# Optimization experiments

Measured on AMD Instinct MI355X. Metric: run time of the kernel, lower is better.

Reference implementation:

```python
import jax, jax.numpy as jnp
import numpy as np

N = 192            # image grid size (NxN)
N_SHOTS = 192
N_SAMPLES = 192
TWO_PI = 2.0 * np.pi
PIPE_ITERS = 3     # gpunufft default is ~10; 3 suffices for a CPU-runnable reference


def initialize_2D_radial(n_shots, n_samples):
    """Radial trajectory, k in [-0.5, 0.5), shape (n_shots*n_samples, 2)."""
    angles = np.pi * np.arange(n_shots) / n_shots
    radii = np.linspace(-0.5, 0.5, n_samples, endpoint=False)
    kx = radii[None, :] * np.cos(angles[:, None])
    ky = radii[None, :] * np.sin(angles[:, None])
    return np.stack([kx, ky], axis=-1).reshape(-1, 2).astype(np.float32)


def setup_inputs() -> dict:
    key = jax.random.key(0)
    x = jax.random.normal(key, (2, N, N), dtype=jnp.float32)  # real/imag image
    trajectory = jnp.asarray(initialize_2D_radial(N_SHOTS, N_SAMPLES))  # (M,2)
    return {"x": x, "trajectory": trajectory}


def _mats(traj):
    # Separable NDFT factors: exp(-2pi i k_x * px), exp(-2pi i k_y * py).
    # A: (M, N), B: (M, N); M*N complex64 ~= 57 MB each.
    p = jnp.arange(N, dtype=jnp.float32) - N / 2.0  # centered pixel coords
    A = jnp.exp(-1j * TWO_PI * traj[:, 0:1] * p[None, :])
    B = jnp.exp(-1j * TWO_PI * traj[:, 1:2] * p[None, :])
    return A.astype(jnp.complex64), B.astype(jnp.complex64)


def _op(img, A, B):
    # type-2 NUFFT (exact NDFT): image (N,N) -> kspace (M,)
    t = jnp.einsum('my,xy->mx', B, img)      # contract y first
    return jnp.einsum('mx,mx->m', A, t)


def _adj(d, A, B):
    # type-1 NUFFT adjoint: samples (M,) -> image (N,N)
    return jnp.einsum('mx,my->xy', jnp.conj(A) * d[:, None], jnp.conj(B))


def _pipe_density(A, B):
    # Pipe & Menon iterative density compensation: w <- w / |F F^H w|
    w = jnp.ones(A.shape[0], dtype=jnp.complex64)
    def body(i, w):
        q = _op(_adj(w, A, B), A, B)
        return w / jnp.maximum(jnp.abs(q), 1e-20)
    w = jax.lax.fori_loop(0, PIPE_ITERS, body, w)
    return jnp.abs(w)  # real positive weights


def reference(x, trajectory):
    img = (x[0] + 1j * x[1]).astype(jnp.complex64)  # (N,N) complex image
    A, B = _mats(trajectory)
    # density weights computed from detached trajectory (gpunufft init-time)
    traj_sg = jax.lax.stop_gradient(trajectory)
    Asg, Bsg = _mats(traj_sg)
    w = jax.lax.stop_gradient(_pipe_density(Asg, Bsg))
    kspace = _op(img, A, B)                       # forward NUFFT
    adjoint = _adj(w * kspace, A, B)              # density-compensated adjoint
    return jnp.stack([adjoint.real, adjoint.imag])  # (2,N,N) float32
```

## Files before the change

kernel.cpp:

```cpp
#include <hip/hip_runtime.h>
#include <math.h>


#define MTOT 36864
#define NPIX 192
#define SPLITS 128
#define MPS (MTOT / SPLITS)
#define ADJ_CHUNKS (MPS / 16)
#define PG 4

typedef __attribute__((ext_vector_type(8))) short s16x8;
typedef __attribute__((ext_vector_type(4))) float f32x4;
typedef __attribute__((ext_vector_type(4))) unsigned u32x4;

__device__ __forceinline__ f32x4 mfma_bf16(u32x4 a, u32x4 b, f32x4 c) {
    return __builtin_amdgcn_mfma_f32_16x16x32_bf16(
        __builtin_bit_cast(s16x8, a), __builtin_bit_cast(s16x8, b), c, 0, 0, 0);
}

__device__ __forceinline__ void split_pk(float a, float b, unsigned &hi, unsigned &lo) {
    const unsigned ua = __float_as_uint(a), ub = __float_as_uint(b);
    const unsigned ha = (ua + 0x8000u) & 0xffff0000u;
    const unsigned hb = (ub + 0x8000u) & 0xffff0000u;
    hi = (ha >> 16) | hb;
    const float la = a - __uint_as_float(ha);
    const float lb = b - __uint_as_float(hb);
    lo = ((__float_as_uint(la) + 0x8000u) >> 16) |
         ((__float_as_uint(lb) + 0x8000u) & 0xffff0000u);
}

__device__ __forceinline__ void ksplit(float k, float &kh, float &kl) {
    kh = __uint_as_float(__float_as_uint(k) & 0xfffff000u);
    kl = k - kh;
}
__device__ __forceinline__ float redphase(float kh, float kl, float p) {
    float r = kh * p;
    r -= rintf(r);
    r = fmaf(kl, p, r);
    return r;
}
__device__ __forceinline__ unsigned rot16(unsigned v) {
    return __builtin_amdgcn_alignbit(v, v, 16);
}

__global__ void precompP_k(const float* __restrict__ traj, const int comp,
                           unsigned* __restrict__ PS) {
    const int m = blockIdx.x * 256 + threadIdx.x;
    const int c = blockIdx.y;
    float kh, kl; ksplit(traj[2 * m + comp], kh, kl);
    const float ph = redphase(kh, kl, (float)(c - 96));
    const float co = __builtin_amdgcn_cosf(ph);
    const float si = __builtin_amdgcn_sinf(ph);
    unsigned h, l; split_pk(co, -si, h, l);
    const int mc = m >> 4, mi = m & 15;
    PS[(size_t)mc * 6144 + c * 16 + mi]        = h;
    PS[(size_t)mc * 6144 + 3072 + c * 16 + mi] = l;
}

__global__ void ebuild_k(const float* __restrict__ traj,
                         const float* __restrict__ dr, const float* __restrict__ di,
                         unsigned* __restrict__ ES) {
    const int m = blockIdx.x * 256 + threadIdx.x;
    const int c = blockIdx.y;
    float kh, kl; ksplit(traj[2 * m], kh, kl);
    const float ph = redphase(kh, kl, (float)(c - 96));
    const float co = __builtin_amdgcn_cosf(ph);
    const float si = __builtin_amdgcn_sinf(ph);
    const float dr_ = dr[m], di_ = di[m];
    const float Er = co * dr_ - si * di_;
    const float Ei = co * di_ + si * dr_;
    unsigned h, l; split_pk(Er, Ei, h, l);
    const int mc = m >> 4, mi = m & 15;
    ES[(size_t)mc * 6144 + c * 16 + mi]        = h;
    ES[(size_t)mc * 6144 + 3072 + c * 16 + mi] = l;
}

__global__ void winit_k(float* __restrict__ wr, float* __restrict__ wi) {
    const int m = blockIdx.x * 256 + threadIdx.x;
    wr[m] = 1.f; wi[m] = 0.f;
}

__global__ __launch_bounds__(64, 4) void adj_gemm_k(
    const unsigned* __restrict__ ES, const unsigned* __restrict__ BS,
    float* __restrict__ outP)
{
    const int lane = threadIdx.x & 63;
    const int l15 = lane & 15, qd = lane >> 4;
    const int L = blockIdx.x;
    const int xcd = L & 7, j = L >> 3;
    const int s = xcd * (SPLITS / 8) + j / 36;
    const int r = j % 36;
    const int tile = r >> 2, wid = r & 3;
    const int bx = tile % 3, by = tile / 3;
    const int wi = wid & 1, wj = wid >> 1;
    const int x0 = bx * 64 + wi * 32, y0 = by * 64 + wj * 32;
    float* outRe = outP + (size_t)(s & (PG - 1)) * (2 * MTOT);
    float* outIm = outRe + MTOT;

    const int eo0 = (x0 + l15) * 16 + qd * 4;
    const int eo1 = (x0 + 16 + l15) * 16 + qd * 4;
    const int bo0 = (y0 + l15) * 16 + qd * 4;
    const int bo1 = (y0 + 16 + l15) * 16 + qd * 4;

    const unsigned* Ep = ES + (size_t)(s * ADJ_CHUNKS) * 6144;
    const unsigned* Bp = BS + (size_t)(s * ADJ_CHUNKS) * 6144;

    f32x4 accRe[2][2], accIm[2][2];
    #pragma unroll
    for (int i = 0; i < 2; ++i)
        #pragma unroll
        for (int j2 = 0; j2 < 2; ++j2) {
            accRe[i][j2] = (f32x4){0.f, 0.f, 0.f, 0.f};
            accIm[i][j2] = (f32x4){0.f, 0.f, 0.f, 0.f};
        }

    u32x4 Ra[8], Rb[8];

#define LOADSET(R)                                          \
    R[0] = *(const u32x4*)(Ep + eo0);                       \
    R[1] = *(const u32x4*)(Ep + eo1);                       \
    R[2] = *(const u32x4*)(Ep + 3072 + eo0);                \
    R[3] = *(const u32x4*)(Ep + 3072 + eo1);                \
    R[4] = *(const u32x4*)(Bp + bo0);                       \
    R[5] = *(const u32x4*)(Bp + bo1);                       \
    R[6] = *(const u32x4*)(Bp + 3072 + bo0);                \
    R[7] = *(const u32x4*)(Bp + 3072 + bo1);

#define COMPUTE(R)                                                         \
    {                                                                      \
        _Pragma("unroll")                                                  \
        for (int sj = 0; sj < 2; ++sj) {                                   \
            const u32x4 Ph = R[4 + sj];                                    \
            const u32x4 Pl = R[6 + sj];                                    \
            u32x4 Qh, Ql;                                                  \
            _Pragma("unroll")                                              \
            for (int rr = 0; rr < 4; ++rr) {                               \
                Qh[rr] = rot16(Ph[rr]) ^ 0x00008000u;                      \
                Ql[rr] = rot16(Pl[rr]) ^ 0x00008000u;                      \
            }                                                              \
            _Pragma("unroll")                                              \
            for (int si = 0; si < 2; ++si) {                               \
                const u32x4 Eh = R[si];                                    \
                const u32x4 El = R[2 + si];                                \
                accRe[si][sj] = mfma_bf16(Eh, Ph, accRe[si][sj]);          \
                accRe[si][sj] = mfma_bf16(Eh, Pl, accRe[si][sj]);          \
                accRe[si][sj] = mfma_bf16(El, Ph, accRe[si][sj]);          \
                accIm[si][sj] = mfma_bf16(Eh, Qh, accIm[si][sj]);          \
                accIm[si][sj] = mfma_bf16(Eh, Ql, accIm[si][sj]);          \
                accIm[si][sj] = mfma_bf16(El, Qh, accIm[si][sj]);          \
            }                                                              \
        }                                                                  \
    }

    LOADSET(Ra);
    #pragma unroll 1
    for (int it = 0; it < (ADJ_CHUNKS - 2) / 2; ++it) {
        Ep += 6144; Bp += 6144;
        LOADSET(Rb);
        __builtin_amdgcn_sched_barrier(0);
        COMPUTE(Ra);
        Ep += 6144; Bp += 6144;
        LOADSET(Ra);
        __builtin_amdgcn_sched_barrier(0);
        COMPUTE(Rb);
    }
    Ep += 6144; Bp += 6144;
    LOADSET(Rb);
    __builtin_amdgcn_sched_barrier(0);
    COMPUTE(Ra);
    __builtin_amdgcn_sched_barrier(0);
    COMPUTE(Rb);

#undef LOADSET
#undef COMPUTE

    #pragma unroll
    for (int si = 0; si < 2; ++si)
        #pragma unroll
        for (int sj = 0; sj < 2; ++sj)
            #pragma unroll
            for (int rg = 0; rg < 4; ++rg) {
                const int x = x0 + si * 16 + qd * 4 + rg;
                const int y = y0 + sj * 16 + l15;
                atomicAdd(outRe + x * NPIX + y, accRe[si][sj][rg]);
                atomicAdd(outIm + x * NPIX + y, accIm[si][sj][rg]);
            }
}

__device__ __forceinline__ void fw_stage_load(const unsigned* __restrict__ Ghi,
                                              const unsigned* __restrict__ Glo,
                                              int tid, int koff, u32x4 st[3]) {
    #pragma unroll
    for (int j = 0; j < 3; ++j) {
        const int li = tid + j * 576;
        if (li < 1536) {
            const int row = li >> 3, pl = (li >> 2) & 1, qt = li & 3;
            const unsigned* src = pl ? Glo : Ghi;
            st[j] = *(const u32x4*)(src + row * 192 + koff + qt * 4);
        }
    }
}
__device__ __forceinline__ void fw_stage_write(unsigned* sb, int tid, const u32x4 st[3]) {
    #pragma unroll
    for (int j = 0; j < 3; ++j) {
        const int li = tid + j * 576;
        if (li < 1536) {
            const int row = li >> 3, pl = (li >> 2) & 1, qt = li & 3;
            *(u32x4*)(sb + pl * 3840 + row * 20 + qt * 4) = st[j];
        }
    }
}

__global__ __launch_bounds__(576) void fwdq_k(
    const float* __restrict__ traj,
    const unsigned* __restrict__ Ghi, const unsigned* __restrict__ Glo,
    float* __restrict__ wre, float* __restrict__ wim,
    const int mode,
    float* __restrict__ qre, float* __restrict__ qim)
{
    __shared__ unsigned sG[2][2 * 3840];
    const int tid = threadIdx.x;
    const int lane = tid & 63, wid = tid >> 6;
    const int l15 = lane & 15, q = lane >> 4;
    const int m = (blockIdx.x * 9 + wid) * 16 + l15;
    const float2 kk = *(const float2*)(traj + 2 * m);
    float kxh, kxl, kyh, kyl;
    ksplit(kk.x, kxh, kxl);
    ksplit(kk.y, kyh, kyl);

    f32x4 tre[12], tim[12];
    #pragma unroll
    for (int i = 0; i < 12; ++i) {
        tre[i] = (f32x4){0.f, 0.f, 0.f, 0.f};
        tim[i] = (f32x4){0.f, 0.f, 0.f, 0.f};
    }

    float bc, bs;
    { const float ph = redphase(kyh, kyl, (float)(q * 4 - 96)); 
      bc = __builtin_amdgcn_cosf(ph); bs = __builtin_amdgcn_sinf(ph); }
    const float r1c = __builtin_amdgcn_cosf(kk.y), r1s = __builtin_amdgcn_sinf(kk.y);
    float r16c, r16s;
    { float g = kk.y * 16.f; g -= rintf(g);
      r16c = __builtin_amdgcn_cosf(g); r16s = __builtin_amdgcn_sinf(g); }

    u32x4 st[3];
    fw_stage_load(Ghi, Glo, tid, 0, st);
    fw_stage_write(&sG[0][0], tid, st);
    __syncthreads();

    for (int ch = 0; ch < 12; ++ch) {
        if (ch < 11) fw_stage_load(Ghi, Glo, tid, (ch + 1) * 16, st);

        u32x4 Ph, Pl, Qh, Ql;
        {
            float c = bc, s = bs;
            #pragma unroll
            for (int r = 0; r < 4; ++r) {
                unsigned h, l; split_pk(c, s, h, l);
                Ph[r] = h; Pl[r] = l;
                Qh[r] = rot16(h) ^ 0x00008000u;
                Ql[r] = rot16(l) ^ 0x00008000u;
                const float nc = c * r1c - s * r1s, ns = s * r1c + c * r1s;
                c = nc; s = ns;
            }
            const float nbc = bc * r16c - bs * r16s, nbs = bs * r16c + bc * r16s;
            bc = nbc; bs = nbs;
        }

        const unsigned* sb = &sG[ch & 1][0];
        #pragma unroll
        for (int si = 0; si < 12; ++si) {
            const int base = (si * 16 + l15) * 20 + q * 4;
            const u32x4 gh = *(const u32x4*)(sb + base);
            const u32x4 gl = *(const u32x4*)(sb + 3840 + base);
            tre[si] = mfma_bf16(gh, Ph, tre[si]);
            tre[si] = mfma_bf16(gh, Pl, tre[si]);
            tre[si] = mfma_bf16(gl, Ph, tre[si]);
            tim[si] = mfma_bf16(gh, Qh, tim[si]);
            tim[si] = mfma_bf16(gh, Ql, tim[si]);
            tim[si] = mfma_bf16(gl, Qh, tim[si]);
        }

        if (ch < 11) {
            __syncthreads();
            fw_stage_write(&sG[(ch + 1) & 1][0], tid, st);
            __syncthreads();
        }
    }

    float qr = 0.f, qi = 0.f;
    {
        float g = kk.x * 16.f; g -= rintf(g);
        const float rc = __builtin_amdgcn_cosf(g), rs = __builtin_amdgcn_sinf(g);
        #pragma unroll
        for (int rg = 0; rg < 4; ++rg) {
            const float ph = redphase(kxh, kxl, (float)(q * 4 + rg - 96));
            float c = __builtin_amdgcn_cosf(ph), s = __builtin_amdgcn_sinf(ph);
            #pragma unroll
            for (int si = 0; si < 12; ++si) {
                const float tr = tre[si][rg], ti = tim[si][rg];
                qr += c * tr + s * ti;
                qi += c * ti - s * tr;
                const float nc = c * rc - s * rs, ns = s * rc + c * rs;
                c = nc; s = ns;
            }
        }
    }
    qr += __shfl_xor(qr, 16); qi += __shfl_xor(qi, 16);
    qr += __shfl_xor(qr, 32); qi += __shfl_xor(qi, 32);
    if (lane < 16) {
        if (mode == 0) {
            const float den = fmaxf(sqrtf(qr * qr + qi * qi), 1e-20f);
            wre[m] /= den; wim[m] /= den;
        } else {
            const float sc = sqrtf(wre[m] * wre[m] + wim[m] * wim[m]);
            qre[m] = qr * sc; qim[m] = qi * sc;
        }
    }
}

__global__ void presplit_k(const float* __restrict__ re, const float* __restrict__ im,
                           unsigned* __restrict__ Gh, unsigned* __restrict__ Gl) {
    const int e = blockIdx.x * 256 + threadIdx.x;
    unsigned h, l;
    split_pk(re[e], im[e], h, l);
    Gh[e] = h; Gl[e] = l;
}

__global__ void presplitP_k(const float* __restrict__ outP,
                            unsigned* __restrict__ Gh, unsigned* __restrict__ Gl) {
    const int e = blockIdx.x * 256 + threadIdx.x;
    float re = 0.f, im = 0.f;
    #pragma unroll
    for (int g = 0; g < PG; ++g) {
        re += outP[(size_t)g * (2 * MTOT) + e];
        im += outP[(size_t)g * (2 * MTOT) + MTOT + e];
    }
    unsigned h, l;
    split_pk(re, im, h, l);
    Gh[e] = h; Gl[e] = l;
}

__global__ void reduceOut_k(const float* __restrict__ outP, float* __restrict__ out) {
    const int e = blockIdx.x * 256 + threadIdx.x;
    float re = 0.f, im = 0.f;
    #pragma unroll
    for (int g = 0; g < PG; ++g) {
        re += outP[(size_t)g * (2 * MTOT) + e];
        im += outP[(size_t)g * (2 * MTOT) + MTOT + e];
    }
    out[e] = re; out[MTOT + e] = im;
}

extern "C" void kernel_launch(void* const* d_in, const int* in_sizes, int n_in,
                              void* d_out, int out_size, void* d_ws, size_t ws_size,
                              hipStream_t stream)
{
    const float* xin  = (const float*)d_in[0];
    const float* traj = (const float*)d_in[1];
    float* out = (float*)d_out;

    char* pb = (char*)d_ws;
    unsigned* BS = (unsigned*)pb; pb += (size_t)2304 * 6144 * 4;
    unsigned* ES = (unsigned*)pb; pb += (size_t)2304 * 6144 * 4;
    float* outP = (float*)pb; pb += (size_t)PG * 2 * MTOT * 4;
    float* wr   = (float*)pb; pb += MTOT * 4;
    float* wi   = (float*)pb; pb += MTOT * 4;
    float* dre  = (float*)pb; pb += MTOT * 4;
    float* dim_ = (float*)pb; pb += MTOT * 4;
    unsigned* Ghi = (unsigned*)pb; pb += MTOT * 4;
    unsigned* Glo = (unsigned*)pb; pb += MTOT * 4;

    precompP_k<<<dim3(MTOT / 256, NPIX), 256, 0, stream>>>(traj, 1, BS);
    winit_k<<<MTOT / 256, 256, 0, stream>>>(wr, wi);

    for (int it = 0; it < 3; ++it) {
        hipMemsetAsync(outP, 0, (size_t)PG * 2 * MTOT * 4, stream);
        ebuild_k<<<dim3(MTOT / 256, NPIX), 256, 0, stream>>>(traj, wr, wi, ES);
        adj_gemm_k<<<36 * SPLITS, 64, 0, stream>>>(ES, BS, outP);
        presplitP_k<<<MTOT / 256, 256, 0, stream>>>(outP, Ghi, Glo);
        fwdq_k<<<256, 576, 0, stream>>>(traj, Ghi, Glo, wr, wi, 0, dre, dim_);
    }

    presplit_k<<<MTOT / 256, 256, 0, stream>>>(xin, xin + MTOT, Ghi, Glo);
    fwdq_k<<<256, 576, 0, stream>>>(traj, Ghi, Glo, wr, wi, 1, dre, dim_);
    hipMemsetAsync(outP, 0, (size_t)PG * 2 * MTOT * 4, stream);
    ebuild_k<<<dim3(MTOT / 256, NPIX), 256, 0, stream>>>(traj, dre, dim_, ES);
    adj_gemm_k<<<36 * SPLITS, 64, 0, stream>>>(ES, BS, outP);
    reduceOut_k<<<MTOT / 256, 256, 0, stream>>>(outP, out);
}
```

Measured before the change: 528.3 us.

## Replace adjoint atomics with per-split partial slabs and drop memsets

```diff
diff --git a/kernel.cpp b/kernel.cpp
--- a/kernel.cpp
+++ b/kernel.cpp
@@ -7,7 +7,7 @@
 #define SPLITS 128
 #define MPS (MTOT / SPLITS)
 #define ADJ_CHUNKS (MPS / 16)
-#define PG 4
+#define PG 128
 
 typedef __attribute__((ext_vector_type(8))) short s16x8;
 typedef __attribute__((ext_vector_type(4))) float f32x4;
@@ -94,13 +94,13 @@
     const int bx = tile % 3, by = tile / 3;
     const int wi = wid & 1, wj = wid >> 1;
     const int x0 = bx * 64 + wi * 32, y0 = by * 64 + wj * 32;
-    float* outRe = outP + (size_t)(s & (PG - 1)) * (2 * MTOT);
+    float* outRe = outP + (size_t)s * (2 * MTOT);
     float* outIm = outRe + MTOT;
 
     const int eo0 = (x0 + l15) * 16 + qd * 4;
-    const int eo1 = (x0 + 16 + l15) * 16 + qd * 4;
+    const int eo1 = eo0 + 256;
     const int bo0 = (y0 + l15) * 16 + qd * 4;
-    const int bo1 = (y0 + 16 + l15) * 16 + qd * 4;
+    const int bo1 = bo0 + 256;
 
     const unsigned* Ep = ES + (size_t)(s * ADJ_CHUNKS) * 6144;
     const unsigned* Bp = BS + (size_t)(s * ADJ_CHUNKS) * 6144;
@@ -114,65 +114,42 @@
             accIm[i][j2] = (f32x4){0.f, 0.f, 0.f, 0.f};
         }
 
-    u32x4 Ra[8], Rb[8];
-
-#define LOADSET(R)                                          \
-    R[0] = *(const u32x4*)(Ep + eo0);                       \
-    R[1] = *(const u32x4*)(Ep + eo1);                       \
-    R[2] = *(const u32x4*)(Ep + 3072 + eo0);                \
-    R[3] = *(const u32x4*)(Ep + 3072 + eo1);                \
-    R[4] = *(const u32x4*)(Bp + bo0);                       \
-    R[5] = *(const u32x4*)(Bp + bo1);                       \
-    R[6] = *(const u32x4*)(Bp + 3072 + bo0);                \
-    R[7] = *(const u32x4*)(Bp + 3072 + bo1);
-
-#define COMPUTE(R)                                                         \
-    {                                                                      \
-        _Pragma("unroll")                                                  \
-        for (int sj = 0; sj < 2; ++sj) {                                   \
-            const u32x4 Ph = R[4 + sj];                                    \
-            const u32x4 Pl = R[6 + sj];                                    \
-            u32x4 Qh, Ql;                                                  \
-            _Pragma("unroll")                                              \
-            for (int rr = 0; rr < 4; ++rr) {                               \
-                Qh[rr] = rot16(Ph[rr]) ^ 0x00008000u;                      \
-                Ql[rr] = rot16(Pl[rr]) ^ 0x00008000u;                      \
-            }                                                              \
-            _Pragma("unroll")                                              \
-            for (int si = 0; si < 2; ++si) {                               \
-                const u32x4 Eh = R[si];                                    \
-                const u32x4 El = R[2 + si];                                \
-                accRe[si][sj] = mfma_bf16(Eh, Ph, accRe[si][sj]);          \
-                accRe[si][sj] = mfma_bf16(Eh, Pl, accRe[si][sj]);          \
-                accRe[si][sj] = mfma_bf16(El, Ph, accRe[si][sj]);          \
-                accIm[si][sj] = mfma_bf16(Eh, Qh, accIm[si][sj]);          \
-                accIm[si][sj] = mfma_bf16(Eh, Ql, accIm[si][sj]);          \
-                accIm[si][sj] = mfma_bf16(El, Qh, accIm[si][sj]);          \
-            }                                                              \
-        }                                                                  \
-    }
-
-    LOADSET(Ra);
     #pragma unroll 1
-    for (int it = 0; it < (ADJ_CHUNKS - 2) / 2; ++it) {
+    for (int ch = 0; ch < ADJ_CHUNKS; ++ch) {
+        const u32x4 Eh0 = *(const u32x4*)(Ep + eo0);
+        const u32x4 Eh1 = *(const u32x4*)(Ep + eo1);
+        const u32x4 El0 = *(const u32x4*)(Ep + 3072 + eo0);
+        const u32x4 El1 = *(const u32x4*)(Ep + 3072 + eo1);
+        const u32x4 Ph0 = *(const u32x4*)(Bp + bo0);
+        const u32x4 Ph1 = *(const u32x4*)(Bp + bo1);
+        const u32x4 Pl0 = *(const u32x4*)(Bp + 3072 + bo0);
+        const u32x4 Pl1 = *(const u32x4*)(Bp + 3072 + bo1);
+        __builtin_amdgcn_sched_barrier(0);
+
+        #pragma unroll
+        for (int sj = 0; sj < 2; ++sj) {
+            const u32x4 Ph = sj ? Ph1 : Ph0;
+            const u32x4 Pl = sj ? Pl1 : Pl0;
+            u32x4 Qh, Ql;
+            #pragma unroll
+            for (int rr = 0; rr < 4; ++rr) {
+                Qh[rr] = rot16(Ph[rr]) ^ 0x00008000u;
+                Ql[rr] = rot16(Pl[rr]) ^ 0x00008000u;
+            }
+            #pragma unroll
+            for (int si = 0; si < 2; ++si) {
+                const u32x4 Eh = si ? Eh1 : Eh0;
+                const u32x4 El = si ? El1 : El0;
+                accRe[si][sj] = mfma_bf16(Eh, Ph, accRe[si][sj]);
+                accRe[si][sj] = mfma_bf16(Eh, Pl, accRe[si][sj]);
+                accRe[si][sj] = mfma_bf16(El, Ph, accRe[si][sj]);
+                accIm[si][sj] = mfma_bf16(Eh, Qh, accIm[si][sj]);
+                accIm[si][sj] = mfma_bf16(Eh, Ql, accIm[si][sj]);
+                accIm[si][sj] = mfma_bf16(El, Qh, accIm[si][sj]);
+            }
+        }
         Ep += 6144; Bp += 6144;
-        LOADSET(Rb);
-        __builtin_amdgcn_sched_barrier(0);
-        COMPUTE(Ra);
-        Ep += 6144; Bp += 6144;
-        LOADSET(Ra);
-        __builtin_amdgcn_sched_barrier(0);
-        COMPUTE(Rb);
-    }
-    Ep += 6144; Bp += 6144;
-    LOADSET(Rb);
-    __builtin_amdgcn_sched_barrier(0);
-    COMPUTE(Ra);
-    __builtin_amdgcn_sched_barrier(0);
-    COMPUTE(Rb);
-
-#undef LOADSET
-#undef COMPUTE
+    }
 
     #pragma unroll
     for (int si = 0; si < 2; ++si)
@@ -182,8 +159,8 @@
             for (int rg = 0; rg < 4; ++rg) {
                 const int x = x0 + si * 16 + qd * 4 + rg;
                 const int y = y0 + sj * 16 + l15;
-                atomicAdd(outRe + x * NPIX + y, accRe[si][sj][rg]);
-                atomicAdd(outIm + x * NPIX + y, accIm[si][sj][rg]);
+                outRe[x * NPIX + y] = accRe[si][sj][rg];
+                outIm[x * NPIX + y] = accIm[si][sj][rg];
             }
 }
 
@@ -331,7 +308,7 @@
                             unsigned* __restrict__ Gh, unsigned* __restrict__ Gl) {
     const int e = blockIdx.x * 256 + threadIdx.x;
     float re = 0.f, im = 0.f;
-    #pragma unroll
+    #pragma unroll 8
     for (int g = 0; g < PG; ++g) {
         re += outP[(size_t)g * (2 * MTOT) + e];
         im += outP[(size_t)g * (2 * MTOT) + MTOT + e];
@@ -344,7 +321,7 @@
 __global__ void reduceOut_k(const float* __restrict__ outP, float* __restrict__ out) {
     const int e = blockIdx.x * 256 + threadIdx.x;
     float re = 0.f, im = 0.f;
-    #pragma unroll
+    #pragma unroll 8
     for (int g = 0; g < PG; ++g) {
         re += outP[(size_t)g * (2 * MTOT) + e];
         im += outP[(size_t)g * (2 * MTOT) + MTOT + e];
@@ -375,7 +352,6 @@
     winit_k<<<MTOT / 256, 256, 0, stream>>>(wr, wi);
 
     for (int it = 0; it < 3; ++it) {
-        hipMemsetAsync(outP, 0, (size_t)PG * 2 * MTOT * 4, stream);
         ebuild_k<<<dim3(MTOT / 256, NPIX), 256, 0, stream>>>(traj, wr, wi, ES);
         adj_gemm_k<<<36 * SPLITS, 64, 0, stream>>>(ES, BS, outP);
         presplitP_k<<<MTOT / 256, 256, 0, stream>>>(outP, Ghi, Glo);
@@ -384,7 +360,6 @@
 
     presplit_k<<<MTOT / 256, 256, 0, stream>>>(xin, xin + MTOT, Ghi, Glo);
     fwdq_k<<<256, 576, 0, stream>>>(traj, Ghi, Glo, wr, wi, 1, dre, dim_);
-    hipMemsetAsync(outP, 0, (size_t)PG * 2 * MTOT * 4, stream);
     ebuild_k<<<dim3(MTOT / 256, NPIX), 256, 0, stream>>>(traj, dre, dim_, ES);
     adj_gemm_k<<<36 * SPLITS, 64, 0, stream>>>(ES, BS, outP);
     reduceOut_k<<<MTOT / 256, 256, 0, stream>>>(outP, out);
```

Measured after the change: 509.0 us. -3.6%, faster.
